# Kernel optimization log

Measured on AMD Instinct MI355X. Metric: run time of the kernel, lower is better.

The kernel has to match this reference:

```python
import jax, jax.numpy as jnp
import numpy as np

B, T, S = 4, 128, 8192
HID, NH, NKV, HD = 2560, 8, 4, 256
INTER = 10240
WINDOW = 1024
SOFTCAP = 50.0
SCALING = 256 ** -0.5  # query_pre_attn_scalar ** -0.5
EPS = 1e-6
NEG = -2.3819763e38  # large negative for masking (matches Gemma mask value)
ROPE_THETA = 10000.0


def _rmsnorm(x, w):
    xf = x.astype(jnp.float32)
    o = xf * jax.lax.rsqrt(jnp.mean(xf * xf, axis=-1, keepdims=True) + EPS)
    return (o * (1.0 + w.astype(jnp.float32))).astype(x.dtype)


def _rope(x, cos, sin):
    # split-half rotation, matching torch apply_rotary_emb (chunk->complex->mul)
    d2 = x.shape[-1] // 2
    x1, x2 = x[..., :d2], x[..., d2:]
    c = cos[None, :, None, :]  # [1,T,1,D/2]
    s = sin[None, :, None, :]
    return jnp.concatenate([x1 * c - x2 * s, x1 * s + x2 * c], axis=-1)


def setup_inputs() -> dict:
    key = jax.random.key(0)
    ks = jax.random.split(key, 14)
    hidden_states = jax.random.normal(ks[0], (B, T, HID), jnp.float32)
    kv_write_indices = jnp.arange(T, dtype=jnp.int32)
    k_cache = jnp.zeros((B, S, NKV, HD), jnp.float32)
    v_cache = jnp.zeros((B, S, NKV, HD), jnp.float32)
    # rotary tables for positions 0..T-1
    inv = 1.0 / (ROPE_THETA ** (np.arange(0, HD, 2)[: HD // 2].astype(np.float32) / HD))
    fr = np.outer(np.arange(T, dtype=np.float32), inv).astype(np.float32)
    freqs_cos = jnp.asarray(np.cos(fr))
    freqs_sin = jnp.asarray(np.sin(fr))
    # masks: query i sits at absolute position i; cache slots >= T are unwritten
    qpos = jnp.arange(T)[:, None]
    kpos = jnp.arange(S)[None, :]
    causal = kpos <= qpos
    local = causal & ((qpos - kpos) < WINDOW)
    mask = jnp.broadcast_to(jnp.where(causal, 0.0, NEG)[None, None], (B, 1, T, S)).astype(jnp.float32)
    local_mask = jnp.broadcast_to(jnp.where(local, 0.0, NEG)[None, None], (B, 1, T, S)).astype(jnp.float32)
    sc = 0.02
    w_qkv = sc * jax.random.normal(ks[1], ((NH + 2 * NKV) * HD, HID), jnp.float32)
    w_o = sc * jax.random.normal(ks[2], (HID, NH * HD), jnp.float32)
    q_norm_w = 0.1 * jax.random.normal(ks[3], (HD,), jnp.float32)
    k_norm_w = 0.1 * jax.random.normal(ks[4], (HD,), jnp.float32)
    in_ln_w = 0.1 * jax.random.normal(ks[5], (HID,), jnp.float32)
    post_attn_ln_w = 0.1 * jax.random.normal(ks[6], (HID,), jnp.float32)
    pre_ffw_ln_w = 0.1 * jax.random.normal(ks[7], (HID,), jnp.float32)
    post_ffw_ln_w = 0.1 * jax.random.normal(ks[8], (HID,), jnp.float32)
    w_gate = sc * jax.random.normal(ks[9], (INTER, HID), jnp.float32)
    w_up = sc * jax.random.normal(ks[10], (INTER, HID), jnp.float32)
    w_down = sc * jax.random.normal(ks[11], (HID, INTER), jnp.float32)
    return {
        "hidden_states": hidden_states, "freqs_cos": freqs_cos, "freqs_sin": freqs_sin,
        "kv_write_indices": kv_write_indices, "k_cache": k_cache, "v_cache": v_cache,
        "mask": mask, "local_mask": local_mask,
        "w_qkv": w_qkv, "w_o": w_o, "q_norm_w": q_norm_w, "k_norm_w": k_norm_w,
        "in_ln_w": in_ln_w, "post_attn_ln_w": post_attn_ln_w,
        "pre_ffw_ln_w": pre_ffw_ln_w, "post_ffw_ln_w": post_ffw_ln_w,
        "w_gate": w_gate, "w_up": w_up, "w_down": w_down,
    }


def reference(hidden_states, freqs_cos, freqs_sin, kv_write_indices, k_cache, v_cache,
              mask, local_mask, w_qkv, w_o, q_norm_w, k_norm_w, in_ln_w,
              post_attn_ln_w, pre_ffw_ln_w, post_ffw_ln_w, w_gate, w_up, w_down):
    b, t, _ = hidden_states.shape
    residual = hidden_states
    h = _rmsnorm(hidden_states, in_ln_w)
    qkv = h @ w_qkv.T
    q_sz, kv_sz = NH * HD, NKV * HD
    xq = qkv[..., :q_sz].reshape(b, t, NH, HD)
    xk = qkv[..., q_sz:q_sz + kv_sz].reshape(b, t, NKV, HD)
    xv = qkv[..., q_sz + kv_sz:].reshape(b, t, NKV, HD)
    xq = _rmsnorm(xq, q_norm_w)  # QK-norm
    xk = _rmsnorm(xk, k_norm_w)
    xq = _rope(xq, freqs_cos, freqs_sin)
    xk = _rope(xk, freqs_cos, freqs_sin)
    kc = k_cache.at[:, kv_write_indices].set(xk)  # index_copy_ on dim 1
    vc = v_cache.at[:, kv_write_indices].set(xv)
    g = NH // NKV
    q = (xq * SCALING).reshape(b, t, NKV, g, HD)
    # GQA without repeat_interleave: group dim g shares each kv head
    scores = jnp.einsum('btkgd,bskd->bkgts', q, kc)
    scores = SOFTCAP * jnp.tanh(scores / SOFTCAP)  # logit softcapping
    scores = scores + local_mask[:, :, None]  # LOCAL_SLIDING -> use local mask
    probs = jax.nn.softmax(scores.astype(jnp.float32), axis=-1).astype(q.dtype)
    attn = jnp.einsum('bkgts,bskd->btkgd', probs, vc).reshape(b, t, NH * HD)
    attn = attn @ w_o.T
    h = residual + _rmsnorm(attn, post_attn_ln_w)
    residual = h
    x = _rmsnorm(h, pre_ffw_ln_w)
    gate = jax.nn.gelu(x @ w_gate.T, approximate=True)
    mlp = (gate * (x @ w_up.T)) @ w_down.T
    return residual + _rmsnorm(mlp, post_ffw_ln_w)
```

## Files before the change

### kernel.cpp

```cpp
#include <hip/hip_runtime.h>
#include <hip/hip_bf16.h>

#define B_ 4
#define T_ 128
#define HID 2560
#define NH 8
#define NKV 4
#define HD 256
#define INTER 10240
#define MROWS 512
#define EPS 1e-6f

typedef float f32x4 __attribute__((ext_vector_type(4)));
typedef __bf16 bf16x8 __attribute__((ext_vector_type(8)));

__device__ __forceinline__ unsigned short f2bf(float f){
  unsigned int u = __builtin_bit_cast(unsigned int, f);
  u += 0x7fffu + ((u >> 16) & 1u);
  return (unsigned short)(u >> 16);
}
__device__ __forceinline__ float bf2f(unsigned short u){
  unsigned int x = ((unsigned int)u) << 16;
  return __builtin_bit_cast(float, x);
}
__device__ __forceinline__ unsigned int cvtpk(float lo, float hi){
  unsigned int r;
  asm("v_cvt_pk_bf16_f32 %0, %1, %2" : "=v"(r) : "v"(lo), "v"(hi));
  return r;
}

__device__ __forceinline__ float bsum256(float v, float* buf){
  #pragma unroll
  for (int o = 32; o; o >>= 1) v += __shfl_xor(v, o);
  __syncthreads();
  if ((threadIdx.x & 63) == 0) buf[threadIdx.x >> 6] = v;
  __syncthreads();
  return buf[0] + buf[1] + buf[2] + buf[3];
}


__global__ __launch_bounds__(256) void rms_in(
    const float* __restrict__ x, const float* __restrict__ w,
    unsigned short* __restrict__ out)
{
  __shared__ float buf[4];
  const int r = blockIdx.x, tid = threadIdx.x;
  const float* xp = x + (size_t)r * HID;
  float v[10]; float ss = 0.f;
  #pragma unroll
  for (int j = 0; j < 10; j++){ v[j] = xp[tid + j*256]; ss += v[j]*v[j]; }
  ss = bsum256(ss, buf);
  float s = rsqrtf(ss * (1.f/HID) + EPS);
  #pragma unroll
  for (int j = 0; j < 10; j++){
    int i = tid + j*256;
    out[((size_t)(i >> 5) * MROWS + r) * 32 + (i & 31)] = f2bf(v[j] * s * (1.f + w[i]));
  }
}

__global__ __launch_bounds__(256, 2) void gemm_big(
    const unsigned short* __restrict__ Ap,
    const float* __restrict__ B0,
    const float* __restrict__ B1,
    int n_hi,
    unsigned short* __restrict__ C,
    int N, int K, int klen, int split_major)
{
  __shared__ char Bs[2][128*64];
  const int tid = threadIdx.x;
  int bid, split;
  if (split_major) {
    int rid = blockIdx.x;
    int i = rid & 7, t2 = rid >> 3;
    split = i*2 + (t2 & 1);
    bid = t2 >> 1;
  } else {
    bid = (blockIdx.x & 7) * ((int)gridDim.x >> 3) + (blockIdx.x >> 3);
    split = blockIdx.y;
  }
  const int bm = (bid & 1) << 8;
  const int bn = (bid >> 1) << 7;
  const int kt0 = (split * klen) >> 5;
  const int nt = klen >> 5;

  const int srow = tid >> 1, shalf = tid & 1;
  const float* Bb = (bn < n_hi) ? B0 : B1;
  const int bnr = (bn < n_hi) ? bn : (bn - n_hi);
  const float* BpG = Bb + (size_t)(bnr + srow) * K + (kt0 << 5) + (shalf << 4);

  const int wave = tid >> 6, lane = tid & 63;
  const int wm = (wave & 1) << 7;
  const int wn = (wave >> 1) << 6;
  const int fr = lane & 15, kq = lane >> 4;
  const int bslot = ((kq ^ ((fr >> 1) & 3)) << 4);
  const int brsw = (srow >> 1) & 3;
  const int s0 = (((2*shalf)     ^ brsw) << 4);
  const int s1 = (((2*shalf + 1) ^ brsw) << 4);

  const unsigned short* ApL = Ap + ((size_t)kt0 * MROWS + bm + wm + fr) * 32 + kq * 8;

  f32x4 acc[8][4];
  #pragma unroll
  for (int i = 0; i < 8; i++)
    #pragma unroll
    for (int j = 0; j < 4; j++)
      #pragma unroll
      for (int e = 0; e < 4; e++) acc[i][j][e] = 0.f;

  uint4 aR[8], aS[8];
  float4 rb0, rb1, rb2, rb3, sb0, sb1, sb2, sb3;

#define ISSUE_A(dst, tt) { const unsigned short* ap = ApL + (size_t)(tt) * 16384; \
  dst[0] = *(const uint4*)(ap);        dst[1] = *(const uint4*)(ap + 512); \
  dst[2] = *(const uint4*)(ap + 1024); dst[3] = *(const uint4*)(ap + 1536); \
  dst[4] = *(const uint4*)(ap + 2048); dst[5] = *(const uint4*)(ap + 2560); \
  dst[6] = *(const uint4*)(ap + 3072); dst[7] = *(const uint4*)(ap + 3584); }
#define LOAD_B(p0,p1,p2,p3, tt) { const float* bp = BpG + ((tt) << 5); \
  p0 = *(const float4*)(bp);     p1 = *(const float4*)(bp + 4); \
  p2 = *(const float4*)(bp + 8); p3 = *(const float4*)(bp + 12); }
#define WRITE_B(cur, b0,b1,b2,b3) { uint4 w0, w1; \
  w0.x = cvtpk(b0.x,b0.y); w0.y = cvtpk(b0.z,b0.w); \
  w0.z = cvtpk(b1.x,b1.y); w0.w = cvtpk(b1.z,b1.w); \
  w1.x = cvtpk(b2.x,b2.y); w1.y = cvtpk(b2.z,b2.w); \
  w1.z = cvtpk(b3.x,b3.y); w1.w = cvtpk(b3.z,b3.w); \
  char* bbase = &Bs[cur][srow*64]; \
  *(uint4*)(bbase + s0) = w0; \
  *(uint4*)(bbase + s1) = w1; }
#define BAR() { asm volatile("s_waitcnt lgkmcnt(0)" ::: "memory"); \
  __builtin_amdgcn_s_barrier(); }
#define COMPUTE(cur, aset) { const char* bb = Bs[cur]; \
  bf16x8 bfv[4]; \
  _Pragma("unroll") for (int ni = 0; ni < 4; ni++) \
    bfv[ni] = *(const bf16x8*)(bb + ((wn + ni*16 + fr) << 6) + bslot); \
  __builtin_amdgcn_s_setprio(1); \
  _Pragma("unroll") for (int mi = 0; mi < 8; mi++){ \
    bf16x8 af = __builtin_bit_cast(bf16x8, aset[mi]); \
    _Pragma("unroll") for (int ni = 0; ni < 4; ni++) \
      acc[mi][ni] = __builtin_amdgcn_mfma_f32_16x16x32_bf16(af, bfv[ni], acc[mi][ni], 0, 0, 0); } \
  __builtin_amdgcn_s_setprio(0); }

  ISSUE_A(aR, 0);
  LOAD_B(rb0,rb1,rb2,rb3, 0);
  LOAD_B(sb0,sb1,sb2,sb3, 1);

  for (int t = 0; t < nt; t += 2) {
    ISSUE_A(aS, t + 1);
    WRITE_B(0, rb0,rb1,rb2,rb3);
    BAR();
    if (t + 2 < nt) LOAD_B(rb0,rb1,rb2,rb3, t + 2);
    COMPUTE(0, aR);
    if (t + 2 < nt) ISSUE_A(aR, t + 2);
    WRITE_B(1, sb0,sb1,sb2,sb3);
    BAR();
    if (t + 3 < nt) LOAD_B(sb0,sb1,sb2,sb3, t + 3);
    COMPUTE(1, aS);
  }
#undef ISSUE_A
#undef LOAD_B
#undef WRITE_B
#undef BAR
#undef COMPUTE

  unsigned short* Cp = C + (size_t)split * MROWS * N;
  #pragma unroll
  for (int mi = 0; mi < 8; mi++) {
    #pragma unroll
    for (int ni = 0; ni < 4; ni++) {
      int m = bm + wm + mi*16 + kq*4;
      int n = bn + wn + ni*16 + fr;
      #pragma unroll
      for (int i = 0; i < 4; i++)
        Cp[(size_t)(m + i) * N + n] = f2bf(acc[mi][ni][i]);
    }
  }
}

__global__ __launch_bounds__(64) void qkv_post(
    const unsigned short* __restrict__ qkvp,
    const float* __restrict__ fcos, const float* __restrict__ fsin,
    const float* __restrict__ qnw, const float* __restrict__ knw,
    float* __restrict__ qout, float* __restrict__ kT, float* __restrict__ vout)
{
  const int row = blockIdx.x;
  const int hh  = blockIdx.y;
  const int b = row >> 7, t = row & 127;
  const int l = threadIdx.x;
  const size_t MS = (size_t)MROWS * 4096;
  const unsigned short* src = qkvp + (size_t)row * 4096 + hh * 256;
  float x[4];
  #pragma unroll
  for (int j = 0; j < 4; j++){
    int d = l + j*64;
    float v = 0.f;
    #pragma unroll
    for (int s = 0; s < 8; s++) v += bf2f(src[d + s*MS]);
    x[j] = v;
  }
  if (hh >= 12) {
    float* vp = vout + ((size_t)(b*NKV + (hh-12)) * T_ + t) * HD;
    #pragma unroll
    for (int j = 0; j < 4; j++) vp[l + j*64] = x[j];
    return;
  }
  float ss = x[0]*x[0] + x[1]*x[1] + x[2]*x[2] + x[3]*x[3];
  #pragma unroll
  for (int o = 32; o; o >>= 1) ss += __shfl_xor(ss, o);
  float r = rsqrtf(ss * (1.f/HD) + EPS);
  const float* nw = (hh < 8) ? qnw : knw;
  #pragma unroll
  for (int j = 0; j < 4; j++){ int d = l + j*64; x[j] = x[j] * r * (1.f + nw[d]); }
  float c0 = fcos[t*128 + l],      s0 = fsin[t*128 + l];
  float c1 = fcos[t*128 + l + 64], s1 = fsin[t*128 + l + 64];
  float y0 = x[0]*c0 - x[2]*s0;
  float y2 = x[0]*s0 + x[2]*c0;
  float y1 = x[1]*c1 - x[3]*s1;
  float y3 = x[1]*s1 + x[3]*c1;
  if (hh < 8) {
    float* qp = qout + ((size_t)(b*NH + hh) * T_ + t) * HD;
    const float sc = 0.0625f;
    qp[l] = y0*sc; qp[l+64] = y1*sc; qp[l+128] = y2*sc; qp[l+192] = y3*sc;
  } else {
    float* kp = kT + (size_t)(b*NKV + (hh-8)) * HD * T_;
    kp[(size_t)(l)*T_ + t] = y0;  kp[(size_t)(l+64)*T_ + t] = y1;
    kp[(size_t)(l+128)*T_ + t] = y2; kp[(size_t)(l+192)*T_ + t] = y3;
  }
}

__global__ __launch_bounds__(128) void attn_fwd(
    const float* __restrict__ q, const float* __restrict__ kT,
    const float* __restrict__ V, unsigned short* __restrict__ att)
{
  const int id = blockIdx.x;
  const int t = id & 127;
  const int h = (id >> 7) & 7;
  const int b = id >> 10;
  const int kvh = h >> 1;
  const int tid = threadIdx.x;
  __shared__ float qs[256];
  __shared__ float sc[128];
  __shared__ float red[128];
  const float* qp = q + (size_t)id * HD;
  qs[tid] = qp[tid]; qs[tid + 128] = qp[tid + 128];
  __syncthreads();
  const float* kp = kT + (size_t)(b*NKV + kvh) * HD * T_;
  float dot = 0.f;
  const bool valid = (tid <= t);
  if (valid) {
    #pragma unroll 8
    for (int d = 0; d < 256; d++) dot += qs[d] * kp[(size_t)d*T_ + tid];
  }
  float score = valid ? 50.f * tanhf(dot * 0.02f) : -3.0e38f;
  sc[tid] = score; red[tid] = score;
  __syncthreads();
  for (int o = 64; o; o >>= 1){ if (tid < o) red[tid] = fmaxf(red[tid], red[tid+o]); __syncthreads(); }
  float m = red[0];
  __syncthreads();
  float p = valid ? __expf(score - m) : 0.f;
  sc[tid] = p; red[tid] = p;
  __syncthreads();
  for (int o = 64; o; o >>= 1){ if (tid < o) red[tid] += red[tid+o]; __syncthreads(); }
  float inv = 1.f / red[0];
  const float* vp = V + (size_t)(b*NKV + kvh) * T_ * HD;
  float a0 = 0.f, a1 = 0.f;
  for (int s = 0; s <= t; s++){
    float ps = sc[s];
    a0 += ps * vp[(size_t)s*HD + tid];
    a1 += ps * vp[(size_t)s*HD + tid + 128];
  }
  const int row = b*T_ + t;
  const int c0 = h*256 + tid, c1 = c0 + 128;
  att[((size_t)(c0 >> 5) * MROWS + row) * 32 + (c0 & 31)] = f2bf(a0 * inv);
  att[((size_t)(c1 >> 5) * MROWS + row) * 32 + (c1 & 31)] = f2bf(a1 * inv);
}

__global__ __launch_bounds__(256) void post_attn_k(
    const unsigned short* __restrict__ op, const float* __restrict__ hs,
    const float* __restrict__ wpost, const float* __restrict__ wpre,
    float* __restrict__ h2, unsigned short* __restrict__ xout)
{
  __shared__ float buf[4];
  const int r = blockIdx.x, tid = threadIdx.x;
  const size_t MS = (size_t)MROWS * HID;
  float o[10]; float ss = 0.f;
  #pragma unroll
  for (int j = 0; j < 10; j++){
    size_t i = (size_t)r*HID + tid + j*256;
    float v = 0.f;
    #pragma unroll
    for (int s = 0; s < 16; s++) v += bf2f(op[i + s*MS]);
    o[j] = v; ss += v*v;
  }
  ss = bsum256(ss, buf);
  float s = rsqrtf(ss*(1.f/HID) + EPS);
  float h[10]; float s2 = 0.f;
  #pragma unroll
  for (int j = 0; j < 10; j++){
    int i = tid + j*256;
    float hv = hs[(size_t)r*HID + i] + o[j]*s*(1.f + wpost[i]);
    h[j] = hv; h2[(size_t)r*HID + i] = hv; s2 += hv*hv;
  }
  s2 = bsum256(s2, buf);
  float sc2 = rsqrtf(s2*(1.f/HID) + EPS);
  #pragma unroll
  for (int j = 0; j < 10; j++){
    int i = tid + j*256;
    xout[((size_t)(i >> 5) * MROWS + r) * 32 + (i & 31)] = f2bf(h[j]*sc2*(1.f + wpre[i]));
  }
}

__global__ __launch_bounds__(256) void act_fuse(
    const unsigned short* __restrict__ gu,
    unsigned short* __restrict__ act)
{
  const int r = blockIdx.x;
  const int c0 = blockIdx.y * 2560;
  const size_t MS = (size_t)MROWS * 20480;
  const unsigned short* rowp = gu + (size_t)r * 20480;
  for (int c = c0 + threadIdx.x; c < c0 + 2560; c += 256){
    float g = 0.f, u = 0.f;
    #pragma unroll
    for (int s = 0; s < 4; s++){
      g += bf2f(rowp[s*MS + c]);
      u += bf2f(rowp[s*MS + c + INTER]);
    }
    float tt = tanhf(0.7978845608f * (g + 0.044715f * g*g*g));
    float ge = 0.5f * g * (1.f + tt);
    act[((size_t)(c >> 5) * MROWS + r) * 32 + (c & 31)] = f2bf(ge * u);
  }
}

__global__ __launch_bounds__(256) void final_k(
    const unsigned short* __restrict__ dp, const float* __restrict__ h2,
    const float* __restrict__ w, float* __restrict__ out)
{
  __shared__ float buf[4];
  const int r = blockIdx.x, tid = threadIdx.x;
  const size_t MS = (size_t)MROWS * HID;
  float m[10]; float ss = 0.f;
  #pragma unroll
  for (int j = 0; j < 10; j++){
    size_t i = (size_t)r*HID + tid + j*256;
    float v = 0.f;
    #pragma unroll
    for (int s = 0; s < 16; s++) v += bf2f(dp[i + s*MS]);
    m[j] = v; ss += v*v;
  }
  ss = bsum256(ss, buf);
  float s = rsqrtf(ss*(1.f/HID) + EPS);
  #pragma unroll
  for (int j = 0; j < 10; j++){
    int i = tid + j*256;
    out[(size_t)r*HID + i] = h2[(size_t)r*HID + i] + m[j]*s*(1.f + w[i]);
  }
}

extern "C" void kernel_launch(void* const* d_in, const int* in_sizes, int n_in,
                              void* d_out, int out_size, void* d_ws, size_t ws_size,
                              hipStream_t stream)
{
  const float* hs     = (const float*)d_in[0];
  const float* fcos   = (const float*)d_in[1];
  const float* fsin   = (const float*)d_in[2];
  const float* w_qkv  = (const float*)d_in[8];
  const float* w_o    = (const float*)d_in[9];
  const float* qnw    = (const float*)d_in[10];
  const float* knw    = (const float*)d_in[11];
  const float* in_ln  = (const float*)d_in[12];
  const float* w_post = (const float*)d_in[13];
  const float* w_pre  = (const float*)d_in[14];
  const float* w_pffw = (const float*)d_in[15];
  const float* w_gate = (const float*)d_in[16];
  const float* w_up   = (const float*)d_in[17];
  const float* w_down = (const float*)d_in[18];
  float* out = (float*)d_out;

  char* p = (char*)d_ws;
  auto alloc = [&](size_t bytes)->void*{ void* r = p; p += (bytes + 255) & ~(size_t)255; return r; };
  void* P0 = alloc((size_t)4*MROWS*20480*2);
  void* P1 = alloc((size_t)16*MROWS*HID*2);
  unsigned short* h_b   = (unsigned short*)alloc((size_t)MROWS*HID*2);
  float* qbuf           = (float*)alloc((size_t)B_*NH*T_*HD*4);
  float* kT             = (float*)alloc((size_t)B_*NKV*HD*T_*4);
  float* vbuf           = (float*)alloc((size_t)B_*NKV*T_*HD*4);
  unsigned short* att_b = (unsigned short*)alloc((size_t)MROWS*2048*2);
  float* h2             = (float*)alloc((size_t)MROWS*HID*4);
  unsigned short* x_b   = (unsigned short*)alloc((size_t)MROWS*HID*2);
  unsigned short* act_b = (unsigned short*)alloc((size_t)MROWS*INTER*2);

  unsigned short* qkv_p = (unsigned short*)P0;
  unsigned short* gu_p  = (unsigned short*)P0;
  unsigned short* o_p   = (unsigned short*)P1;
  unsigned short* down_p= (unsigned short*)P1;

  rms_in<<<MROWS, 256, 0, stream>>>(hs, in_ln, h_b);
  gemm_big<<<dim3(64, 8), 256, 0, stream>>>(h_b, w_qkv, w_qkv, 1<<30, qkv_p, 4096, 2560, 320, 0);
  qkv_post<<<dim3(MROWS, 16), 64, 0, stream>>>(qkv_p, fcos, fsin, qnw, knw, qbuf, kT, vbuf);
  attn_fwd<<<B_*NH*T_, 128, 0, stream>>>(qbuf, kT, vbuf, att_b);
  gemm_big<<<dim3(40, 16), 256, 0, stream>>>(att_b, w_o, w_o, 1<<30, o_p, 2560, 2048, 128, 0);
  post_attn_k<<<MROWS, 256, 0, stream>>>(o_p, hs, w_post, w_pre, h2, x_b);
  gemm_big<<<dim3(320, 4), 256, 0, stream>>>(x_b, w_gate, w_up, 10240, gu_p, 20480, 2560, 640, 0);
  act_fuse<<<dim3(MROWS, 4), 256, 0, stream>>>(gu_p, act_b);
  gemm_big<<<640, 256, 0, stream>>>(act_b, w_down, w_down, 1<<30, down_p, 2560, 10240, 640, 1);
  final_k<<<MROWS, 256, 0, stream>>>(down_p, h2, w_pffw, out);
}
```

Measured before the change: 345.5 us.

## Stream fp32 weight tiles to LDS via direct global-to-LDS loads with 64-wide K

Rewrites the GEMM mainloop so fp32 weight tiles are copied straight into LDS with global_load_lds (XOR-swizzled), and converted to bf16 when read from LDS instead of passing through registers. The K step per iteration doubles to 64, and B tiles are double-buffered with one barrier pair per iteration. The o-projection split count is halved to match, and post_attn reduces 8 partials. LDS use per block grows fourfold (64KB), which may lower occupancy, and the A loads are no longer prefetched a step ahead.

```diff
diff --git a/kernel.cpp b/kernel.cpp
--- a/kernel.cpp
+++ b/kernel.cpp
@@ -28,6 +28,11 @@
   asm("v_cvt_pk_bf16_f32 %0, %1, %2" : "=v"(r) : "v"(lo), "v"(hi));
   return r;
 }
+__device__ __forceinline__ void glds16(const void* g, void* l){
+  __builtin_amdgcn_global_load_lds(
+      (const __attribute__((address_space(1))) void*)g,
+      (__attribute__((address_space(3))) void*)l, 16, 0, 0);
+}
 
 __device__ __forceinline__ float bsum256(float v, float* buf){
   #pragma unroll
@@ -66,7 +71,7 @@
     unsigned short* __restrict__ C,
     int N, int K, int klen, int split_major)
 {
-  __shared__ char Bs[2][128*64];
+  __shared__ char Bs[2][128*256];
   const int tid = threadIdx.x;
   int bid, split;
   if (split_major) {
@@ -80,24 +85,18 @@
   }
   const int bm = (bid & 1) << 8;
   const int bn = (bid >> 1) << 7;
-  const int kt0 = (split * klen) >> 5;
-  const int nt = klen >> 5;
-
-  const int srow = tid >> 1, shalf = tid & 1;
+  const int kt0 = (split * klen) >> 6;
+  const int nt = klen >> 6;
+
+  const int w = tid >> 6, l = tid & 63;
   const float* Bb = (bn < n_hi) ? B0 : B1;
   const int bnr = (bn < n_hi) ? bn : (bn - n_hi);
-  const float* BpG = Bb + (size_t)(bnr + srow) * K + (kt0 << 5) + (shalf << 4);
-
-  const int wave = tid >> 6, lane = tid & 63;
-  const int wm = (wave & 1) << 7;
-  const int wn = (wave >> 1) << 6;
-  const int fr = lane & 15, kq = lane >> 4;
-  const int bslot = ((kq ^ ((fr >> 1) & 3)) << 4);
-  const int brsw = (srow >> 1) & 3;
-  const int s0 = (((2*shalf)     ^ brsw) << 4);
-  const int s1 = (((2*shalf + 1) ^ brsw) << 4);
-
-  const unsigned short* ApL = Ap + ((size_t)kt0 * MROWS + bm + wm + fr) * 32 + kq * 8;
+
+  const int wm = (w & 1) << 7;
+  const int wn = (w >> 1) << 6;
+  const int fr = l & 15, kq = l >> 4;
+
+  const unsigned short* ApL = Ap + ((size_t)(kt0*2) * MROWS + bm + wm + fr) * 32 + kq * 8;
 
   f32x4 acc[8][4];
   #pragma unroll
@@ -107,59 +106,77 @@
       #pragma unroll
       for (int e = 0; e < 4; e++) acc[i][j][e] = 0.f;
 
-  uint4 aR[8], aS[8];
-  float4 rb0, rb1, rb2, rb3, sb0, sb1, sb2, sb3;
-
-#define ISSUE_A(dst, tt) { const unsigned short* ap = ApL + (size_t)(tt) * 16384; \
-  dst[0] = *(const uint4*)(ap);        dst[1] = *(const uint4*)(ap + 512); \
-  dst[2] = *(const uint4*)(ap + 1024); dst[3] = *(const uint4*)(ap + 1536); \
-  dst[4] = *(const uint4*)(ap + 2048); dst[5] = *(const uint4*)(ap + 2560); \
-  dst[6] = *(const uint4*)(ap + 3072); dst[7] = *(const uint4*)(ap + 3584); }
-#define LOAD_B(p0,p1,p2,p3, tt) { const float* bp = BpG + ((tt) << 5); \
-  p0 = *(const float4*)(bp);     p1 = *(const float4*)(bp + 4); \
-  p2 = *(const float4*)(bp + 8); p3 = *(const float4*)(bp + 12); }
-#define WRITE_B(cur, b0,b1,b2,b3) { uint4 w0, w1; \
-  w0.x = cvtpk(b0.x,b0.y); w0.y = cvtpk(b0.z,b0.w); \
-  w0.z = cvtpk(b1.x,b1.y); w0.w = cvtpk(b1.z,b1.w); \
-  w1.x = cvtpk(b2.x,b2.y); w1.y = cvtpk(b2.z,b2.w); \
-  w1.z = cvtpk(b3.x,b3.y); w1.w = cvtpk(b3.z,b3.w); \
-  char* bbase = &Bs[cur][srow*64]; \
-  *(uint4*)(bbase + s0) = w0; \
-  *(uint4*)(bbase + s1) = w1; }
-#define BAR() { asm volatile("s_waitcnt lgkmcnt(0)" ::: "memory"); \
-  __builtin_amdgcn_s_barrier(); }
-#define COMPUTE(cur, aset) { const char* bb = Bs[cur]; \
-  bf16x8 bfv[4]; \
-  _Pragma("unroll") for (int ni = 0; ni < 4; ni++) \
-    bfv[ni] = *(const bf16x8*)(bb + ((wn + ni*16 + fr) << 6) + bslot); \
-  __builtin_amdgcn_s_setprio(1); \
+  uint4 ar[16];
+
+#define ISSUE_A(tt) { \
+  const unsigned short* a0 = ApL + (size_t)(2*(tt)) * 16384; \
+  const unsigned short* a1 = a0 + 16384; \
   _Pragma("unroll") for (int mi = 0; mi < 8; mi++){ \
-    bf16x8 af = __builtin_bit_cast(bf16x8, aset[mi]); \
-    _Pragma("unroll") for (int ni = 0; ni < 4; ni++) \
-      acc[mi][ni] = __builtin_amdgcn_mfma_f32_16x16x32_bf16(af, bfv[ni], acc[mi][ni], 0, 0, 0); } \
-  __builtin_amdgcn_s_setprio(0); }
-
-  ISSUE_A(aR, 0);
-  LOAD_B(rb0,rb1,rb2,rb3, 0);
-  LOAD_B(sb0,sb1,sb2,sb3, 1);
-
-  for (int t = 0; t < nt; t += 2) {
-    ISSUE_A(aS, t + 1);
-    WRITE_B(0, rb0,rb1,rb2,rb3);
-    BAR();
-    if (t + 2 < nt) LOAD_B(rb0,rb1,rb2,rb3, t + 2);
-    COMPUTE(0, aR);
-    if (t + 2 < nt) ISSUE_A(aR, t + 2);
-    WRITE_B(1, sb0,sb1,sb2,sb3);
-    BAR();
-    if (t + 3 < nt) LOAD_B(sb0,sb1,sb2,sb3, t + 3);
-    COMPUTE(1, aS);
-  }
+    ar[mi]     = *(const uint4*)(a0 + mi*512*4); \
+    ar[8 + mi] = *(const uint4*)(a1 + mi*512*4); } }
 #undef ISSUE_A
-#undef LOAD_B
-#undef WRITE_B
-#undef BAR
-#undef COMPUTE
+#define ISSUE_A(tt) { \
+  const unsigned short* a0 = ApL + (size_t)(2*(tt)) * 16384; \
+  const unsigned short* a1 = a0 + 16384; \
+  _Pragma("unroll") for (int mi = 0; mi < 8; mi++){ \
+    ar[mi]     = *(const uint4*)(a0 + mi*512); \
+    ar[8 + mi] = *(const uint4*)(a1 + mi*512); } }
+
+#define GLDS_B(tt, slot) { \
+  char* dst = Bs[slot] + (w << 13); \
+  const int kf = (kt0 + (tt)) << 6; \
+  _Pragma("unroll") for (int g = 0; g < 8; g++){ \
+    int row = (w << 5) + (g << 2) + (l >> 4); \
+    int j = (l & 15) ^ (row & 7); \
+    const float* src = Bb + (size_t)(bnr + row) * K + kf + (j << 2); \
+    glds16(src, dst + (g << 10)); } }
+#define VM(n) asm volatile("s_waitcnt vmcnt(" #n ")" ::: "memory")
+#define MIN_(a,b) ((a)<(b)?(a):(b))
+
+  GLDS_B(0, 0);
+  GLDS_B(1, 1);
+
+  for (int t = 0; t < nt; t++) {
+    const int cur = t & 1;
+    ISSUE_A(t);
+    VM(24);
+    bf16x8 bfv[2][4];
+    #pragma unroll
+    for (int kk = 0; kk < 2; kk++){
+      #pragma unroll
+      for (int ni = 0; ni < 4; ni++){
+        int row = wn + ni*16 + fr;
+        const char* rb = Bs[cur] + (row << 8);
+        int c0 = kk*8 + kq*2;
+        int sw = row & 7;
+        f32x4 lo = *(const f32x4*)(rb + (((c0  ) ^ sw) << 4));
+        f32x4 hi = *(const f32x4*)(rb + (((c0+1) ^ sw) << 4));
+        union { unsigned int u[4]; bf16x8 v; } pk;
+        pk.u[0] = cvtpk(lo[0], lo[1]); pk.u[1] = cvtpk(lo[2], lo[3]);
+        pk.u[2] = cvtpk(hi[0], hi[1]); pk.u[3] = cvtpk(hi[2], hi[3]);
+        bfv[kk][ni] = pk.v;
+      }
+    }
+    asm volatile("s_waitcnt lgkmcnt(0)" ::: "memory");
+    __builtin_amdgcn_s_barrier();
+    GLDS_B(MIN_(t+2, nt-1), cur);
+    __builtin_amdgcn_s_setprio(1);
+    #pragma unroll
+    for (int kk = 0; kk < 2; kk++)
+      #pragma unroll
+      for (int mi = 0; mi < 8; mi++){
+        bf16x8 af = __builtin_bit_cast(bf16x8, ar[kk*8 + mi]);
+        #pragma unroll
+        for (int ni = 0; ni < 4; ni++)
+          acc[mi][ni] = __builtin_amdgcn_mfma_f32_16x16x32_bf16(af, bfv[kk][ni], acc[mi][ni], 0, 0, 0);
+      }
+    __builtin_amdgcn_s_setprio(0);
+    __builtin_amdgcn_s_barrier();
+  }
+#undef ISSUE_A
+#undef GLDS_B
+#undef VM
+#undef MIN_
 
   unsigned short* Cp = C + (size_t)split * MROWS * N;
   #pragma unroll
@@ -287,7 +304,7 @@
     size_t i = (size_t)r*HID + tid + j*256;
     float v = 0.f;
     #pragma unroll
-    for (int s = 0; s < 16; s++) v += bf2f(op[i + s*MS]);
+    for (int s = 0; s < 8; s++) v += bf2f(op[i + s*MS]);
     o[j] = v; ss += v*v;
   }
   ss = bsum256(ss, buf);
@@ -396,7 +413,7 @@
   gemm_big<<<dim3(64, 8), 256, 0, stream>>>(h_b, w_qkv, w_qkv, 1<<30, qkv_p, 4096, 2560, 320, 0);
   qkv_post<<<dim3(MROWS, 16), 64, 0, stream>>>(qkv_p, fcos, fsin, qnw, knw, qbuf, kT, vbuf);
   attn_fwd<<<B_*NH*T_, 128, 0, stream>>>(qbuf, kT, vbuf, att_b);
-  gemm_big<<<dim3(40, 16), 256, 0, stream>>>(att_b, w_o, w_o, 1<<30, o_p, 2560, 2048, 128, 0);
+  gemm_big<<<dim3(40, 8), 256, 0, stream>>>(att_b, w_o, w_o, 1<<30, o_p, 2560, 2048, 256, 0);
   post_attn_k<<<MROWS, 256, 0, stream>>>(o_p, hs, w_post, w_pre, h2, x_b);
   gemm_big<<<dim3(320, 4), 256, 0, stream>>>(x_b, w_gate, w_up, 10240, gu_p, 20480, 2560, 640, 0);
   act_fuse<<<dim3(MROWS, 4), 256, 0, stream>>>(gu_p, act_b);
```

Measured after the change: 334.6 us. 3.2% less time.
